# Optimization experiments

Measured on AMD Instinct MI355X. Metric: run time of the kernel, lower is better.

## Reference

```python
import jax, jax.numpy as jnp
import numpy as np

N, C_IN, C_OUT, D, H, T, V = 32, 64, 64, 64, 8, 128, 25
KT, KS = 5, 3  # (time, spatial) kernel sizes
EPS = 1e-5


def pos_embed(C, T, V):
    # sinusoidal positional embedding over flattened (T*V) positions -> (1,C,T,V)
    pos = jnp.arange(T * V, dtype=jnp.float32)[:, None]
    div = jnp.exp(jnp.arange(0, C, 2, dtype=jnp.float32) * (-np.log(10000.0) / C))
    pe = jnp.zeros((T * V, C), dtype=jnp.float32)
    pe = pe.at[:, 0::2].set(jnp.sin(pos * div))
    pe = pe.at[:, 1::2].set(jnp.cos(pos * div))
    return pe.reshape(T, V, C).transpose(2, 0, 1)[None]


def batchnorm(x, gamma, beta):
    # training-mode BatchNorm2d: batch statistics over (N,T,V) per channel
    mean = x.mean(axis=(0, 2, 3), keepdims=True)
    var = x.var(axis=(0, 2, 3), keepdims=True)
    return (x - mean) * jax.lax.rsqrt(var + EPS) * gamma[None, :, None, None] + beta[None, :, None, None]


def conv2d(x, w, b, pad):
    y = jax.lax.conv_general_dilated(x, w, (1, 1), pad, dimension_numbers=('NCHW', 'OIHW', 'NCHW'))
    return y + b[None, :, None, None]


def setup_inputs() -> dict:
    key = jax.random.key(0)
    ks = jax.random.split(key, 12)
    s = 0.05
    return {
        'x': jax.random.normal(ks[0], (N, C_IN, T, V), jnp.float32),
        'W_qkv': jax.random.normal(ks[1], (3 * H * D, C_IN), jnp.float32) * s,
        'b_qkv': jnp.zeros((3 * H * D,), jnp.float32),
        'alphas': jnp.ones((1, H, 1, 1), jnp.float32),
        'att0s': jnp.ones((1, H, V, V), jnp.float32) / V,
        'W_attn_out': jax.random.normal(ks[2], (C_OUT, H * D), jnp.float32) * s,
        'b_attn_out': jnp.zeros((C_OUT,), jnp.float32),
        'W_spatial': jax.random.normal(ks[3], (C_OUT, C_OUT, 1, KS), jnp.float32) * s,
        'b_spatial': jnp.zeros((C_OUT,), jnp.float32),
        'W_time': jax.random.normal(ks[4], (C_OUT, C_OUT, KT, 1), jnp.float32) * s,
        'b_time': jnp.zeros((C_OUT,), jnp.float32),
        'gamma': jnp.ones((C_OUT,), jnp.float32),
        'beta': jnp.zeros((C_OUT,), jnp.float32),
    }


def reference(x, W_qkv, b_qkv, alphas, att0s, W_attn_out, b_attn_out,
              W_spatial, b_spatial, W_time, b_time, gamma, beta):
    n = x.shape[0]
    xs = x + pos_embed(C_IN, T, V)
    # 1x1 conv QKV projection: (N, 3*H*D, T, V)
    qkv = jnp.einsum('oc,nctv->notv', W_qkv, xs) + b_qkv[None, :, None, None]
    qkv = qkv.reshape(n, 3, H, D, T, V)
    q, k, v = qkv[:, 0], qkv[:, 1], qkv[:, 2]
    # joint-joint attention scores, contracting channel & time; scale T/sqrt(D)
    scores = jnp.einsum('nhctv,nhctu->nhuv', q, k) * (T / np.sqrt(D))
    probs = jnp.tanh(scores) * alphas + att0s  # tanh gating + learnable bias
    att = jnp.einsum('nhuv,nhctv->nhctu', probs, v).reshape(n, H * D, T, V)
    att = jnp.einsum('oc,nctv->notv', W_attn_out, att) + b_attn_out[None, :, None, None]
    residual = x  # in_channels == out_channels -> identity residual_proj
    xs2 = conv2d(att, W_spatial, b_spatial, [(0, 0), (KS // 2, KS // 2)])
    xs2 = jax.nn.relu(batchnorm(xs2, gamma, beta) + residual)
    xt = conv2d(xs2, W_time, b_time, [(KT // 2, KT // 2), (0, 0)])
    xt = jax.nn.relu(batchnorm(xt, gamma, beta) + residual)
    return xt
```

## Files before the change

kernel.cpp:

```cpp
#include <hip/hip_runtime.h>
#include <hip/hip_bf16.h>
#include <math.h>

constexpr int N_  = 32;
constexpr int C_  = 64;
constexpr int T_  = 128;
constexpr int V_  = 25;
constexpr int TV  = T_ * V_;
constexpr float NTV = 102400.0f;

constexpr size_t OFF_MT    = 0;
constexpr size_t OFF_P     = 32768;
constexpr size_t OFF_ZB    = 65536;
constexpr size_t OFF_MK    = 66048;
constexpr size_t OFF_MQ    = 66560;
constexpr size_t OFF_S0    = 67072;
constexpr size_t OFF_WSP   = 67136;
constexpr size_t OFF_WT    = 79424;
constexpr size_t OFF_SG    = 99904;
constexpr size_t OFF_RU    = 259904;
constexpr size_t OFF_RV    = 266304;
constexpr size_t OFF_PROBS = 272704;
constexpr size_t OFF_ST1   = 432704;
constexpr size_t OFF_ST2   = 432832;
constexpr size_t OFF_AB1   = 432960;
constexpr size_t OFF_AB2   = 433088;
constexpr size_t OFF_XS    = 433216;
constexpr size_t OFF_Y2    = OFF_XS;

#define LOAD25(dst, base)                                                     \
  { const float4* _p4 = (const float4*)(base);                                \
    float4 _a = _p4[0], _b = _p4[1], _c = _p4[2], _d = _p4[3], _e = _p4[4],   \
           _f = _p4[5];                                                       \
    dst[0]=_a.x; dst[1]=_a.y; dst[2]=_a.z; dst[3]=_a.w;                       \
    dst[4]=_b.x; dst[5]=_b.y; dst[6]=_b.z; dst[7]=_b.w;                       \
    dst[8]=_c.x; dst[9]=_c.y; dst[10]=_c.z; dst[11]=_c.w;                     \
    dst[12]=_d.x; dst[13]=_d.y; dst[14]=_d.z; dst[15]=_d.w;                   \
    dst[16]=_e.x; dst[17]=_e.y; dst[18]=_e.z; dst[19]=_e.w;                   \
    dst[20]=_f.x; dst[21]=_f.y; dst[22]=_f.z; dst[23]=_f.w;                   \
    dst[24]=((const float*)(base))[24]; }

#define STORE25(base, src)                                                    \
  { float4* _p4 = (float4*)(base);                                           \
    _p4[0] = make_float4(src[0],src[1],src[2],src[3]);                        \
    _p4[1] = make_float4(src[4],src[5],src[6],src[7]);                        \
    _p4[2] = make_float4(src[8],src[9],src[10],src[11]);                      \
    _p4[3] = make_float4(src[12],src[13],src[14],src[15]);                    \
    _p4[4] = make_float4(src[16],src[17],src[18],src[19]);                    \
    _p4[5] = make_float4(src[20],src[21],src[22],src[23]);                    \
    ((float*)(base))[24] = src[24]; }

__global__ void k_xs(const float* __restrict__ x, float* __restrict__ ws) {
    int i4 = blockIdx.x * 256 + threadIdx.x;
    int row = i4 / 800;
    int q = i4 % 800;
    int c = row & 63;
    int r0 = q * 4;
    float f = __expf(-(float)(2 * (c >> 1)) * 0.14391156816875288f);
    float4 xv = ((const float4*)x)[i4];
    float a0 = r0 * f, a1 = (r0 + 1) * f, a2 = (r0 + 2) * f, a3 = (r0 + 3) * f;
    float4 r;
    if (c & 1) {
        r.x = xv.x + __cosf(a0); r.y = xv.y + __cosf(a1);
        r.z = xv.z + __cosf(a2); r.w = xv.w + __cosf(a3);
    } else {
        r.x = xv.x + __sinf(a0); r.y = xv.y + __sinf(a1);
        r.z = xv.z + __sinf(a2); r.w = xv.w + __sinf(a3);
    }
    ((float4*)(ws + OFF_XS))[i4] = r;
}

__global__ void k_setup(const float* __restrict__ Wqkv, const float* __restrict__ bqkv,
                        const float* __restrict__ Wao, const float* __restrict__ Wsp,
                        const float* __restrict__ Wt, float* __restrict__ ws) {
    int i = blockIdx.x * 256 + threadIdx.x;
    if (i < 32768) {
        int h = i >> 12, c = (i >> 6) & 63, cp = i & 63;
        const float* wk = Wqkv + (size_t)(512 + h * 64) * 64;
        const float* wq = Wqkv + (size_t)(h * 64) * 64;
        float s = 0.f;
        for (int dd = 0; dd < 64; ++dd) s = fmaf(wk[dd * 64 + cp], wq[dd * 64 + c], s);
        ws[OFF_MT + i] = s;
        return;
    }
    int j = i - 32768;
    if (j < 32768) {
        int h = j >> 12, c = (j >> 6) & 63, o = j & 63;
        const float* wa = Wao + (size_t)o * 512 + h * 64;
        const float* wv = Wqkv + (size_t)(1024 + h * 64) * 64;
        float s = 0.f;
        for (int dd = 0; dd < 64; ++dd) s = fmaf(wa[dd], wv[dd * 64 + c], s);
        ws[OFF_P + j] = s;
        return;
    }
    j -= 32768;
    if (j < 512) {
        int h = j >> 6, o = j & 63;
        float s = 0.f;
        for (int dd = 0; dd < 64; ++dd)
            s = fmaf(Wao[(size_t)o * 512 + h * 64 + dd], bqkv[1024 + h * 64 + dd], s);
        ws[OFF_ZB + j] = s;
        return;
    }
    j -= 512;
    if (j < 512) {
        int h = j >> 6, cp = j & 63;
        float s = 0.f;
        for (int dd = 0; dd < 64; ++dd)
            s = fmaf(Wqkv[(size_t)(512 + h * 64 + dd) * 64 + cp], bqkv[h * 64 + dd], s);
        ws[OFF_MK + j] = s;
        return;
    }
    j -= 512;
    if (j < 512) {
        int h = j >> 6, c = j & 63;
        float s = 0.f;
        for (int dd = 0; dd < 64; ++dd)
            s = fmaf(Wqkv[(size_t)(h * 64 + dd) * 64 + c], bqkv[512 + h * 64 + dd], s);
        ws[OFF_MQ + j] = s;
        return;
    }
    j -= 512;
    if (j < 8) {
        float s = 0.f;
        for (int dd = 0; dd < 64; ++dd) s = fmaf(bqkv[j * 64 + dd], bqkv[512 + j * 64 + dd], s);
        ws[OFF_S0 + j] = s;
        return;
    }
    j -= 8;
    if (j < 12288) {
        int tap = j >> 12, rest = j & 4095, c = rest >> 6, o = rest & 63;
        ws[OFF_WSP + j] = Wsp[(size_t)o * 192 + c * 3 + tap];
        return;
    }
    j -= 12288;
    if (j < 20480) {
        int kt = j >> 12, rest = j & 4095, c = rest >> 6, o = rest & 63;
        ws[OFF_WT + j] = Wt[(size_t)o * 320 + c * 5 + kt];
        return;
    }
}

__global__ __launch_bounds__(256) void k_scores(float* __restrict__ ws) {
    __shared__ float Mt[64][64];
    __shared__ float G[4][64][28];
    __shared__ float A[4][64][28];
    __shared__ float Rs[64][25];
    int nb = blockIdx.x;
    int n = nb >> 5, h = (nb >> 2) & 7, tq = nb & 3;
    int tid = threadIdx.x;
    for (int e = tid; e < 4096; e += 256) Mt[e >> 6][e & 63] = ws[OFF_MT + (size_t)h * 4096 + e];
    for (int e = tid; e < 1600; e += 256) Rs[e / 25][e % 25] = 0.f;
    const float4* xs4 = (const float4*)(ws + OFF_XS + (size_t)n * 64 * 3200);
    int cp = tid & 63;
    int tt = tid >> 6;
    int vB = tid % 25, c0B = (tid / 25) * 8;
    float accB[25];
#pragma unroll
    for (int u = 0; u < 25; ++u) accB[u] = 0.f;

    for (int ch = 0; ch < 8; ++ch) {
        int t0 = tq * 32 + ch * 4;
        __syncthreads();
        for (int e4 = tid; e4 < 1600; e4 += 256) {
            int c = e4 / 25, q = e4 % 25;
            float4 fv = xs4[c * 800 + ((t0 * 25) >> 2) + q];
            int jj = q * 4;
            G[jj / 25][c][jj % 25] = fv.x;
            G[(jj + 1) / 25][c][(jj + 1) % 25] = fv.y;
            G[(jj + 2) / 25][c][(jj + 2) % 25] = fv.z;
            G[(jj + 3) / 25][c][(jj + 3) % 25] = fv.w;
        }
        __syncthreads();
        for (int e = tid; e < 1600; e += 256) {
            int c = e / 25, v = e % 25;
            Rs[c][v] += G[0][c][v] + G[1][c][v] + G[2][c][v] + G[3][c][v];
        }
        float acc[25];
#pragma unroll
        for (int u = 0; u < 25; ++u) acc[u] = 0.f;
        for (int c = 0; c < 64; ++c) {
            float m = Mt[c][cp];
            float gx[25];
            LOAD25(gx, G[tt][c]);
#pragma unroll
            for (int u = 0; u < 25; ++u) acc[u] = fmaf(m, gx[u], acc[u]);
        }
        STORE25(A[tt][cp], acc);
        __syncthreads();
        if (tid < 200) {
            for (int ci = 0; ci < 8; ++ci) {
                int c = c0B + ci;
#pragma unroll
                for (int t2 = 0; t2 < 4; ++t2) {
                    float av = A[t2][c][vB];
                    float gx[25];
                    LOAD25(gx, G[t2][c]);
#pragma unroll
                    for (int u = 0; u < 25; ++u) accB[u] = fmaf(gx[u], av, accB[u]);
                }
            }
        }
    }
    __syncthreads();
    float* Sl = &G[0][0][0];
    for (int e = tid; e < 640; e += 256) Sl[e] = 0.f;
    __syncthreads();
    if (tid < 200) {
#pragma unroll
        for (int u = 0; u < 25; ++u) atomicAdd(&Sl[u * 25 + vB], accB[u]);
    }
    __syncthreads();
    float* sg = ws + OFF_SG + (size_t)(n * 8 + h) * 625;
    for (int e = tid; e < 625; e += 256) atomicAdd(&sg[e], Sl[e]);
    if (tid < 50) {
        int u = tid % 25;
        const float* mw = ws + ((tid < 25) ? OFF_MK : OFF_MQ) + h * 64;
        float s = 0.f;
        for (int c = 0; c < 64; ++c) s = fmaf(mw[c], Rs[c][u], s);
        size_t dst = ((tid < 25) ? OFF_RU : OFF_RV) + (size_t)(n * 8 + h) * 25 + u;
        atomicAdd(&ws[dst], s);
    }
}

__global__ void k_probs(const float* __restrict__ alphas, const float* __restrict__ att0s,
                        float* __restrict__ ws) {
    int i = blockIdx.x * 256 + threadIdx.x;
    int nh = i / 625, uv = i % 625;
    int h = nh & 7, u = uv / 25, v = uv % 25;
    float s = ws[OFF_SG + i] + ws[OFF_RU + nh * 25 + u] + ws[OFF_RV + nh * 25 + v]
            + 128.f * ws[OFF_S0 + h];
    ws[OFF_PROBS + i] = tanhf(16.f * s) * alphas[h] + att0s[h * 625 + uv];
}

__global__ __launch_bounds__(256) void k_att(const float* __restrict__ bao,
                                             const float* __restrict__ bsp,
                                             float* __restrict__ y1,
                                             float* __restrict__ ws) {
    __shared__ float XS[4][64][28];
    __shared__ float WT[64][64];
    __shared__ float PRT[25][28];
    __shared__ float red[2][4][64];
    int nb = blockIdx.x;
    int n = nb >> 5, tc = nb & 31;
    int tid = threadIdx.x;
    int o = tid & 63, tl = tid >> 6;
    const float4* xs4 = (const float4*)(ws + OFF_XS + (size_t)n * 64 * 3200);
    for (int e4 = tid; e4 < 1600; e4 += 256) {
        int c = e4 / 25, q = e4 % 25;
        float4 fv = xs4[c * 800 + tc * 25 + q];
        int jj = q * 4;
        XS[jj / 25][c][jj % 25] = fv.x;
        XS[(jj + 1) / 25][c][(jj + 1) % 25] = fv.y;
        XS[(jj + 2) / 25][c][(jj + 2) % 25] = fv.z;
        XS[(jj + 3) / 25][c][(jj + 3) % 25] = fv.w;
    }
    const float* pg = ws + OFF_PROBS + (size_t)n * 8 * 625;
    float acc[25];
    float bv = bao[o];
#pragma unroll
    for (int u = 0; u < 25; ++u) acc[u] = bv;

    for (int h = 0; h < 8; ++h) {
        __syncthreads();
        for (int e = tid; e < 4096; e += 256) WT[e >> 6][e & 63] = ws[OFF_P + (size_t)h * 4096 + e];
        for (int e = tid; e < 625; e += 256) PRT[e % 25][e / 25] = pg[h * 625 + e];
        __syncthreads();
        float z[25];
#pragma unroll
        for (int v = 0; v < 25; ++v) z[v] = 0.f;
        for (int c = 0; c < 64; ++c) {
            float w = WT[c][o];
            float gx[25];
            LOAD25(gx, XS[tl][c]);
#pragma unroll
            for (int v = 0; v < 25; ++v) z[v] = fmaf(w, gx[v], z[v]);
        }
        float zb = ws[OFF_ZB + h * 64 + o];
#pragma unroll
        for (int v = 0; v < 25; ++v) z[v] += zb;
        for (int v = 0; v < 25; ++v) {
            float pr[25];
            LOAD25(pr, PRT[v]);
            float zv = z[v];
#pragma unroll
            for (int u = 0; u < 25; ++u) acc[u] = fmaf(zv, pr[u], acc[u]);
        }
    }
    __syncthreads();
    STORE25(XS[tl][o], acc);

    float ca[25];
    float bs = bsp[o];
#pragma unroll
    for (int u = 0; u < 25; ++u) ca[u] = bs;
    for (int j = 0; j < 3; ++j) {
        __syncthreads();
        for (int e = tid; e < 4096; e += 256) WT[e >> 6][e & 63] = ws[OFF_WSP + (size_t)j * 4096 + e];
        __syncthreads();
        for (int c = 0; c < 64; ++c) {
            float w = WT[c][o];
            float gx[25];
            LOAD25(gx, XS[tl][c]);
            if (j == 0) {
#pragma unroll
                for (int u = 1; u < 25; ++u) ca[u] = fmaf(w, gx[u - 1], ca[u]);
            } else if (j == 1) {
#pragma unroll
                for (int u = 0; u < 25; ++u) ca[u] = fmaf(w, gx[u], ca[u]);
            } else {
#pragma unroll
                for (int u = 0; u < 24; ++u) ca[u] = fmaf(w, gx[u + 1], ca[u]);
            }
        }
    }

    float s1 = 0.f, s2 = 0.f;
#pragma unroll
    for (int u = 0; u < 25; ++u) { s1 += ca[u]; s2 = fmaf(ca[u], ca[u], s2); }
    red[0][tl][o] = s1;
    red[1][tl][o] = s2;
    __syncthreads();
    if (tid < 64) {
        float ss = red[0][0][tid] + red[0][1][tid] + red[0][2][tid] + red[0][3][tid];
        float sq = red[1][0][tid] + red[1][1][tid] + red[1][2][tid] + red[1][3][tid];
        atomicAdd(&ws[OFF_ST1 + tid], ss);
        atomicAdd(&ws[OFF_ST1 + 64 + tid], sq);
    }
    float* yb = y1 + (size_t)n * C_ * TV + (size_t)o * TV + (size_t)(tc * 4 + tl) * 25;
#pragma unroll
    for (int u = 0; u < 25; ++u) yb[u] = ca[u];
}

__global__ void k_bn(const float* __restrict__ gamma, const float* __restrict__ beta,
                     float* __restrict__ ws, size_t statoff, size_t aboff) {
    int c = threadIdx.x;
    if (c < 64) {
        float s = ws[statoff + c], sq = ws[statoff + 64 + c];
        float mean = s / NTV;
        float var = sq / NTV - mean * mean;
        float a = gamma[c] / sqrtf(var + 1e-5f);
        ws[aboff + c] = a;
        ws[aboff + 64 + c] = beta[c] - mean * a;
    }
}

__global__ __launch_bounds__(256) void k_time(const float* __restrict__ x,
                                              const float* __restrict__ y1,
                                              const float* __restrict__ bt,
                                              float* __restrict__ ws) {
    __shared__ float XS[8][64][28];
    __shared__ float WT[64][64];
    __shared__ float ab[128];
    __shared__ float red[2][4][64];
    int nb = blockIdx.x;
    int n = nb >> 5;
    int t0 = (nb & 31) * 4;
    int tid = threadIdx.x;
    if (tid < 128) ab[tid] = ws[OFF_AB1 + tid];
    __syncthreads();
    const float* xb = x + (size_t)n * C_ * TV;
    const float* yb = y1 + (size_t)n * C_ * TV;
    for (int e = tid; e < 12800; e += 256) {
        int c = e / 200, s = e % 200;
        int tt = t0 - 2 + s / 25;
        float val = 0.f;
        if (tt >= 0 && tt < 128) {
            size_t idx = (size_t)c * TV + tt * 25 + (s % 25);
            val = fmaxf(fmaf(ab[c], yb[idx], ab[64 + c]) + xb[idx], 0.f);
        }
        XS[s / 25][c][s % 25] = val;
    }
    int o = tid & 63;
    int tl = tid >> 6;
    float acc[25];
    float bv = bt[o];
#pragma unroll
    for (int u = 0; u < 25; ++u) acc[u] = bv;
    for (int kt = 0; kt < 5; ++kt) {
        __syncthreads();
        for (int e = tid; e < 4096; e += 256) WT[e >> 6][e & 63] = ws[OFF_WT + (size_t)kt * 4096 + e];
        __syncthreads();
        for (int c = 0; c < 64; ++c) {
            float w = WT[c][o];
            float gx[25];
            LOAD25(gx, XS[tl + kt][c]);
#pragma unroll
            for (int u = 0; u < 25; ++u) acc[u] = fmaf(w, gx[u], acc[u]);
        }
    }
    float s1 = 0.f, s2 = 0.f;
#pragma unroll
    for (int u = 0; u < 25; ++u) { s1 += acc[u]; s2 = fmaf(acc[u], acc[u], s2); }
    red[0][tl][o] = s1;
    red[1][tl][o] = s2;
    __syncthreads();
    if (tid < 64) {
        float ss = red[0][0][tid] + red[0][1][tid] + red[0][2][tid] + red[0][3][tid];
        float sq = red[1][0][tid] + red[1][1][tid] + red[1][2][tid] + red[1][3][tid];
        atomicAdd(&ws[OFF_ST2 + tid], ss);
        atomicAdd(&ws[OFF_ST2 + 64 + tid], sq);
    }
    float* y2b = ws + OFF_Y2 + (size_t)n * C_ * TV + (size_t)o * TV + (size_t)(t0 + tl) * 25;
#pragma unroll
    for (int u = 0; u < 25; ++u) y2b[u] = acc[u];
}

__global__ void k_final(const float* __restrict__ x, const float* __restrict__ ws,
                        float* __restrict__ out) {
    int i = blockIdx.x * 256 + threadIdx.x;
    if (i < 1638400) {
        const float4* y4 = (const float4*)(ws + OFF_Y2);
        const float4* x4 = (const float4*)x;
        float4 y = y4[i], xx = x4[i];
        int c = (i / 800) & 63;
        float a = ws[OFF_AB2 + c], b = ws[OFF_AB2 + 64 + c];
        float4 r;
        r.x = fmaxf(fmaf(a, y.x, b) + xx.x, 0.f);
        r.y = fmaxf(fmaf(a, y.y, b) + xx.y, 0.f);
        r.z = fmaxf(fmaf(a, y.z, b) + xx.z, 0.f);
        r.w = fmaxf(fmaf(a, y.w, b) + xx.w, 0.f);
        ((float4*)out)[i] = r;
    }
}

extern "C" void kernel_launch(void* const* d_in, const int* in_sizes, int n_in,
                              void* d_out, int out_size, void* d_ws, size_t ws_size,
                              hipStream_t stream) {
    const float* x      = (const float*)d_in[0];
    const float* Wqkv   = (const float*)d_in[1];
    const float* bqkv   = (const float*)d_in[2];
    const float* alphas = (const float*)d_in[3];
    const float* att0s  = (const float*)d_in[4];
    const float* Wao    = (const float*)d_in[5];
    const float* bao    = (const float*)d_in[6];
    const float* Wsp    = (const float*)d_in[7];
    const float* bsp    = (const float*)d_in[8];
    const float* Wt     = (const float*)d_in[9];
    const float* bt     = (const float*)d_in[10];
    const float* gamma  = (const float*)d_in[11];
    const float* beta   = (const float*)d_in[12];
    float* out = (float*)d_out;
    float* ws  = (float*)d_ws;
    float* y1  = out;

    hipMemsetAsync((char*)d_ws + OFF_SG * 4, 0, (160000 + 6400 + 6400) * 4, stream);
    hipMemsetAsync((char*)d_ws + OFF_ST1 * 4, 0, 256 * 4, stream);

    k_xs    <<<dim3(6400), dim3(256), 0, stream>>>(x, ws);
    k_setup <<<dim3(391),  dim3(256), 0, stream>>>(Wqkv, bqkv, Wao, Wsp, Wt, ws);
    k_scores<<<dim3(1024), dim3(256), 0, stream>>>(ws);
    k_probs <<<dim3(625),  dim3(256), 0, stream>>>(alphas, att0s, ws);
    k_att   <<<dim3(1024), dim3(256), 0, stream>>>(bao, bsp, y1, ws);
    k_bn    <<<dim3(1),    dim3(64),  0, stream>>>(gamma, beta, ws, OFF_ST1, OFF_AB1);
    k_time  <<<dim3(1024), dim3(256), 0, stream>>>(x, y1, bt, ws);
    k_bn    <<<dim3(1),    dim3(64),  0, stream>>>(gamma, beta, ws, OFF_ST2, OFF_AB2);
    k_final <<<dim3(6400), dim3(256), 0, stream>>>(x, ws, out);
}
```

Measured before the change: 840.6 us.

## Register-block two output channels per thread and read weights directly from global

Result: faster. 690.7 us (-17.8%).

```diff
diff --git a/kernel.cpp b/kernel.cpp
--- a/kernel.cpp
+++ b/kernel.cpp
@@ -141,20 +141,20 @@
     }
 }
 
-__global__ __launch_bounds__(256) void k_scores(float* __restrict__ ws) {
-    __shared__ float Mt[64][64];
+__global__ __launch_bounds__(256, 2) void k_scores(float* __restrict__ ws) {
     __shared__ float G[4][64][28];
     __shared__ float A[4][64][28];
     __shared__ float Rs[64][25];
     int nb = blockIdx.x;
     int n = nb >> 5, h = (nb >> 2) & 7, tq = nb & 3;
     int tid = threadIdx.x;
-    for (int e = tid; e < 4096; e += 256) Mt[e >> 6][e & 63] = ws[OFF_MT + (size_t)h * 4096 + e];
     for (int e = tid; e < 1600; e += 256) Rs[e / 25][e % 25] = 0.f;
     const float4* xs4 = (const float4*)(ws + OFF_XS + (size_t)n * 64 * 3200);
-    int cp = tid & 63;
+    int cpg = tid & 31, cp0 = cpg * 2;
+    int cs = (tid >> 5) & 1;
     int tt = tid >> 6;
     int vB = tid % 25, c0B = (tid / 25) * 8;
+    const float2* mt2 = (const float2*)(ws + OFF_MT + (size_t)h * 4096);
     float accB[25];
 #pragma unroll
     for (int u = 0; u < 25; ++u) accB[u] = 0.f;
@@ -176,17 +176,31 @@
             int c = e / 25, v = e % 25;
             Rs[c][v] += G[0][c][v] + G[1][c][v] + G[2][c][v] + G[3][c][v];
         }
-        float acc[25];
-#pragma unroll
-        for (int u = 0; u < 25; ++u) acc[u] = 0.f;
-        for (int c = 0; c < 64; ++c) {
-            float m = Mt[c][cp];
+        float a0[25], a1[25];
+#pragma unroll
+        for (int v = 0; v < 25; ++v) { a0[v] = 0.f; a1[v] = 0.f; }
+        for (int ci = 0; ci < 32; ++ci) {
+            int c = cs * 32 + ci;
+            float2 m = mt2[c * 32 + cpg];
             float gx[25];
             LOAD25(gx, G[tt][c]);
 #pragma unroll
-            for (int u = 0; u < 25; ++u) acc[u] = fmaf(m, gx[u], acc[u]);
-        }
-        STORE25(A[tt][cp], acc);
+            for (int v = 0; v < 25; ++v) {
+                a0[v] = fmaf(m.x, gx[v], a0[v]);
+                a1[v] = fmaf(m.y, gx[v], a1[v]);
+            }
+        }
+        if (cs == 1) { STORE25(A[tt][cp0], a0); STORE25(A[tt][cp0 + 1], a1); }
+        __syncthreads();
+        if (cs == 0) {
+            float p0[25], p1[25];
+            LOAD25(p0, A[tt][cp0]);
+            LOAD25(p1, A[tt][cp0 + 1]);
+#pragma unroll
+            for (int v = 0; v < 25; ++v) { a0[v] += p0[v]; a1[v] += p1[v]; }
+            STORE25(A[tt][cp0], a0);
+            STORE25(A[tt][cp0 + 1], a1);
+        }
         __syncthreads();
         if (tid < 200) {
             for (int ci = 0; ci < 8; ++ci) {
@@ -233,22 +247,22 @@
     ws[OFF_PROBS + i] = tanhf(16.f * s) * alphas[h] + att0s[h * 625 + uv];
 }
 
-__global__ __launch_bounds__(256) void k_att(const float* __restrict__ bao,
-                                             const float* __restrict__ bsp,
-                                             float* __restrict__ y1,
-                                             float* __restrict__ ws) {
-    __shared__ float XS[4][64][28];
-    __shared__ float WT[64][64];
+__global__ __launch_bounds__(256, 2) void k_att(const float* __restrict__ bao,
+                                                const float* __restrict__ bsp,
+                                                float* __restrict__ y1,
+                                                float* __restrict__ ws) {
+    __shared__ float XS[8][64][28];
     __shared__ float PRT[25][28];
-    __shared__ float red[2][4][64];
+    __shared__ float red[2][8][64];
     int nb = blockIdx.x;
-    int n = nb >> 5, tc = nb & 31;
+    int n = nb >> 4, tc = nb & 15;
     int tid = threadIdx.x;
-    int o = tid & 63, tl = tid >> 6;
+    int og = tid & 31, o0 = og * 2;
+    int tl = tid >> 5;
     const float4* xs4 = (const float4*)(ws + OFF_XS + (size_t)n * 64 * 3200);
-    for (int e4 = tid; e4 < 1600; e4 += 256) {
-        int c = e4 / 25, q = e4 % 25;
-        float4 fv = xs4[c * 800 + tc * 25 + q];
+    for (int e4 = tid; e4 < 3200; e4 += 256) {
+        int c = e4 / 50, q = e4 % 50;
+        float4 fv = xs4[c * 800 + tc * 50 + q];
         int jj = q * 4;
         XS[jj / 25][c][jj % 25] = fv.x;
         XS[(jj + 1) / 25][c][(jj + 1) % 25] = fv.y;
@@ -256,80 +270,98 @@
         XS[(jj + 3) / 25][c][(jj + 3) % 25] = fv.w;
     }
     const float* pg = ws + OFF_PROBS + (size_t)n * 8 * 625;
-    float acc[25];
-    float bv = bao[o];
-#pragma unroll
-    for (int u = 0; u < 25; ++u) acc[u] = bv;
+    float acc0[25], acc1[25];
+    float b0 = bao[o0], b1 = bao[o0 + 1];
+#pragma unroll
+    for (int u = 0; u < 25; ++u) { acc0[u] = b0; acc1[u] = b1; }
 
     for (int h = 0; h < 8; ++h) {
         __syncthreads();
-        for (int e = tid; e < 4096; e += 256) WT[e >> 6][e & 63] = ws[OFF_P + (size_t)h * 4096 + e];
         for (int e = tid; e < 625; e += 256) PRT[e % 25][e / 25] = pg[h * 625 + e];
         __syncthreads();
-        float z[25];
-#pragma unroll
-        for (int v = 0; v < 25; ++v) z[v] = 0.f;
+        float z0[25], z1[25];
+#pragma unroll
+        for (int v = 0; v < 25; ++v) { z0[v] = 0.f; z1[v] = 0.f; }
+        const float2* pt2 = (const float2*)(ws + OFF_P + (size_t)h * 4096);
         for (int c = 0; c < 64; ++c) {
-            float w = WT[c][o];
+            float2 w = pt2[c * 32 + og];
             float gx[25];
             LOAD25(gx, XS[tl][c]);
 #pragma unroll
-            for (int v = 0; v < 25; ++v) z[v] = fmaf(w, gx[v], z[v]);
-        }
-        float zb = ws[OFF_ZB + h * 64 + o];
-#pragma unroll
-        for (int v = 0; v < 25; ++v) z[v] += zb;
+            for (int v = 0; v < 25; ++v) {
+                z0[v] = fmaf(w.x, gx[v], z0[v]);
+                z1[v] = fmaf(w.y, gx[v], z1[v]);
+            }
+        }
+        float2 zb = ((const float2*)(ws + OFF_ZB + h * 64))[og];
+#pragma unroll
+        for (int v = 0; v < 25; ++v) { z0[v] += zb.x; z1[v] += zb.y; }
         for (int v = 0; v < 25; ++v) {
             float pr[25];
             LOAD25(pr, PRT[v]);
-            float zv = z[v];
-#pragma unroll
-            for (int u = 0; u < 25; ++u) acc[u] = fmaf(zv, pr[u], acc[u]);
-        }
-    }
-    __syncthreads();
-    STORE25(XS[tl][o], acc);
-
-    float ca[25];
-    float bs = bsp[o];
-#pragma unroll
-    for (int u = 0; u < 25; ++u) ca[u] = bs;
+            float zv0 = z0[v], zv1 = z1[v];
+#pragma unroll
+            for (int u = 0; u < 25; ++u) {
+                acc0[u] = fmaf(zv0, pr[u], acc0[u]);
+                acc1[u] = fmaf(zv1, pr[u], acc1[u]);
+            }
+        }
+    }
+    __syncthreads();
+    STORE25(XS[tl][o0], acc0);
+    STORE25(XS[tl][o0 + 1], acc1);
+    __syncthreads();
+
+    float ca0[25], ca1[25];
+    float s0 = bsp[o0], s1_ = bsp[o0 + 1];
+#pragma unroll
+    for (int u = 0; u < 25; ++u) { ca0[u] = s0; ca1[u] = s1_; }
     for (int j = 0; j < 3; ++j) {
-        __syncthreads();
-        for (int e = tid; e < 4096; e += 256) WT[e >> 6][e & 63] = ws[OFF_WSP + (size_t)j * 4096 + e];
-        __syncthreads();
-        for (int c = 0; c < 64; ++c) {
-            float w = WT[c][o];
+        const float2* wsp2 = (const float2*)(ws + OFF_WSP + (size_t)j * 4096);
+        for (int c2 = 0; c2 < 64; ++c2) {
+            float2 w = wsp2[c2 * 32 + og];
             float gx[25];
-            LOAD25(gx, XS[tl][c]);
+            LOAD25(gx, XS[tl][c2]);
             if (j == 0) {
 #pragma unroll
-                for (int u = 1; u < 25; ++u) ca[u] = fmaf(w, gx[u - 1], ca[u]);
+                for (int u = 1; u < 25; ++u) {
+                    ca0[u] = fmaf(w.x, gx[u - 1], ca0[u]);
+                    ca1[u] = fmaf(w.y, gx[u - 1], ca1[u]);
+                }
             } else if (j == 1) {
 #pragma unroll
-                for (int u = 0; u < 25; ++u) ca[u] = fmaf(w, gx[u], ca[u]);
+                for (int u = 0; u < 25; ++u) {
+                    ca0[u] = fmaf(w.x, gx[u], ca0[u]);
+                    ca1[u] = fmaf(w.y, gx[u], ca1[u]);
+                }
             } else {
 #pragma unroll
-                for (int u = 0; u < 24; ++u) ca[u] = fmaf(w, gx[u + 1], ca[u]);
+                for (int u = 0; u < 24; ++u) {
+                    ca0[u] = fmaf(w.x, gx[u + 1], ca0[u]);
+                    ca1[u] = fmaf(w.y, gx[u + 1], ca1[u]);
+                }
             }
         }
     }
 
-    float s1 = 0.f, s2 = 0.f;
-#pragma unroll
-    for (int u = 0; u < 25; ++u) { s1 += ca[u]; s2 = fmaf(ca[u], ca[u], s2); }
-    red[0][tl][o] = s1;
-    red[1][tl][o] = s2;
+    float p1 = 0.f, p2 = 0.f, q1 = 0.f, q2 = 0.f;
+#pragma unroll
+    for (int u = 0; u < 25; ++u) {
+        p1 += ca0[u]; p2 = fmaf(ca0[u], ca0[u], p2);
+        q1 += ca1[u]; q2 = fmaf(ca1[u], ca1[u], q2);
+    }
+    red[0][tl][o0] = p1; red[0][tl][o0 + 1] = q1;
+    red[1][tl][o0] = p2; red[1][tl][o0 + 1] = q2;
     __syncthreads();
     if (tid < 64) {
-        float ss = red[0][0][tid] + red[0][1][tid] + red[0][2][tid] + red[0][3][tid];
-        float sq = red[1][0][tid] + red[1][1][tid] + red[1][2][tid] + red[1][3][tid];
+        float ss = 0.f, sq = 0.f;
+        for (int t2 = 0; t2 < 8; ++t2) { ss += red[0][t2][tid]; sq += red[1][t2][tid]; }
         atomicAdd(&ws[OFF_ST1 + tid], ss);
         atomicAdd(&ws[OFF_ST1 + 64 + tid], sq);
     }
-    float* yb = y1 + (size_t)n * C_ * TV + (size_t)o * TV + (size_t)(tc * 4 + tl) * 25;
-#pragma unroll
-    for (int u = 0; u < 25; ++u) yb[u] = ca[u];
+    float* yb = y1 + (size_t)n * C_ * TV + (size_t)o0 * TV + (size_t)(tc * 8 + tl) * 25;
+#pragma unroll
+    for (int u = 0; u < 25; ++u) { yb[u] = ca0[u]; yb[TV + u] = ca1[u]; }
 }
 
 __global__ void k_bn(const float* __restrict__ gamma, const float* __restrict__ beta,
@@ -345,18 +377,20 @@
     }
 }
 
-__global__ __launch_bounds__(256) void k_time(const float* __restrict__ x,
-                                              const float* __restrict__ y1,
-                                              const float* __restrict__ bt,
-                                              float* __restrict__ ws) {
+__global__ __launch_bounds__(256, 2) void k_time(const float* __restrict__ x,
+                                                 const float* __restrict__ y1,
+                                                 const float* __restrict__ bt,
+                                                 float* __restrict__ ws) {
     __shared__ float XS[8][64][28];
-    __shared__ float WT[64][64];
     __shared__ float ab[128];
     __shared__ float red[2][4][64];
     int nb = blockIdx.x;
     int n = nb >> 5;
     int t0 = (nb & 31) * 4;
     int tid = threadIdx.x;
+    int og = tid & 31, o0 = og * 2;
+    int tl = (tid >> 5) & 3;
+    int cs = tid >> 7;
     if (tid < 128) ab[tid] = ws[OFF_AB1 + tid];
     __syncthreads();
     const float* xb = x + (size_t)n * C_ * TV;
@@ -371,29 +405,45 @@
         }
         XS[s / 25][c][s % 25] = val;
     }
-    int o = tid & 63;
-    int tl = tid >> 6;
-    float acc[25];
-    float bv = bt[o];
-#pragma unroll
-    for (int u = 0; u < 25; ++u) acc[u] = bv;
+    float a0[25], a1[25];
+    float b0 = bt[o0], b1 = bt[o0 + 1];
+#pragma unroll
+    for (int u = 0; u < 25; ++u) { a0[u] = b0; a1[u] = b1; }
+    __syncthreads();
     for (int kt = 0; kt < 5; ++kt) {
-        __syncthreads();
-        for (int e = tid; e < 4096; e += 256) WT[e >> 6][e & 63] = ws[OFF_WT + (size_t)kt * 4096 + e];
-        __syncthreads();
-        for (int c = 0; c < 64; ++c) {
-            float w = WT[c][o];
+        const float2* wt2 = (const float2*)(ws + OFF_WT + (size_t)kt * 4096);
+        for (int ci = 0; ci < 32; ++ci) {
+            int c = cs * 32 + ci;
+            float2 w = wt2[c * 32 + og];
             float gx[25];
             LOAD25(gx, XS[tl + kt][c]);
 #pragma unroll
-            for (int u = 0; u < 25; ++u) acc[u] = fmaf(w, gx[u], acc[u]);
-        }
-    }
-    float s1 = 0.f, s2 = 0.f;
-#pragma unroll
-    for (int u = 0; u < 25; ++u) { s1 += acc[u]; s2 = fmaf(acc[u], acc[u], s2); }
-    red[0][tl][o] = s1;
-    red[1][tl][o] = s2;
+            for (int u = 0; u < 25; ++u) {
+                a0[u] = fmaf(w.x, gx[u], a0[u]);
+                a1[u] = fmaf(w.y, gx[u], a1[u]);
+            }
+        }
+    }
+    __syncthreads();
+    float* comb = &XS[0][0][0];
+    int slot = tid & 127;
+    if (cs == 1) { STORE25(comb + slot * 56, a0); STORE25(comb + slot * 56 + 28, a1); }
+    __syncthreads();
+    if (cs == 0) {
+        float p0[25], p1v[25];
+        LOAD25(p0, comb + slot * 56);
+        LOAD25(p1v, comb + slot * 56 + 28);
+#pragma unroll
+        for (int u = 0; u < 25; ++u) { a0[u] += p0[u]; a1[u] += p1v[u]; }
+        float s1 = 0.f, s2 = 0.f, t1 = 0.f, t2v = 0.f;
+#pragma unroll
+        for (int u = 0; u < 25; ++u) {
+            s1 += a0[u]; s2 = fmaf(a0[u], a0[u], s2);
+            t1 += a1[u]; t2v = fmaf(a1[u], a1[u], t2v);
+        }
+        red[0][tl][o0] = s1; red[0][tl][o0 + 1] = t1;
+        red[1][tl][o0] = s2; red[1][tl][o0 + 1] = t2v;
+    }
     __syncthreads();
     if (tid < 64) {
         float ss = red[0][0][tid] + red[0][1][tid] + red[0][2][tid] + red[0][3][tid];
@@ -401,9 +451,11 @@
         atomicAdd(&ws[OFF_ST2 + tid], ss);
         atomicAdd(&ws[OFF_ST2 + 64 + tid], sq);
     }
-    float* y2b = ws + OFF_Y2 + (size_t)n * C_ * TV + (size_t)o * TV + (size_t)(t0 + tl) * 25;
-#pragma unroll
-    for (int u = 0; u < 25; ++u) y2b[u] = acc[u];
+    if (cs == 0) {
+        float* y2b = ws + OFF_Y2 + (size_t)n * C_ * TV + (size_t)o0 * TV + (size_t)(t0 + tl) * 25;
+#pragma unroll
+        for (int u = 0; u < 25; ++u) { y2b[u] = a0[u]; y2b[TV + u] = a1[u]; }
+    }
 }
 
 __global__ void k_final(const float* __restrict__ x, const float* __restrict__ ws,
@@ -451,7 +503,7 @@
     k_setup <<<dim3(391),  dim3(256), 0, stream>>>(Wqkv, bqkv, Wao, Wsp, Wt, ws);
     k_scores<<<dim3(1024), dim3(256), 0, stream>>>(ws);
     k_probs <<<dim3(625),  dim3(256), 0, stream>>>(alphas, att0s, ws);
-    k_att   <<<dim3(1024), dim3(256), 0, stream>>>(bao, bsp, y1, ws);
+    k_att   <<<dim3(512),  dim3(256), 0, stream>>>(bao, bsp, y1, ws);
     k_bn    <<<dim3(1),    dim3(64),  0, stream>>>(gamma, beta, ws, OFF_ST1, OFF_AB1);
     k_time  <<<dim3(1024), dim3(256), 0, stream>>>(x, y1, bt, ws);
     k_bn    <<<dim3(1),    dim3(64),  0, stream>>>(gamma, beta, ws, OFF_ST2, OFF_AB2);
```
